# Kernel optimization log

Hardware: AMD Instinct MI355X
Metric: run time of the kernel (lower is better)

The kernel has to match this reference:

```python
import jax, jax.numpy as jnp
import numpy as np

B = 4096
D = 1024
WEIGHT = 1.0
EPS = 1e-7  # Keras K.epsilon()


def setup_inputs() -> dict:
    key = jax.random.key(0)
    k1, k2 = jax.random.split(key)
    return {
        "left": jax.random.normal(k1, (B, D), dtype=jnp.float32),
        "right": jax.random.normal(k2, (B, D), dtype=jnp.float32),
        "temperature": jnp.zeros((1,), dtype=jnp.float32),
    }


def _l2_normalize(x):
    # matches l2_norm: sqrt(max(sum(x^2), eps))
    sq = jnp.sum(jnp.square(x), axis=-1, keepdims=True)
    return x / jnp.sqrt(jnp.maximum(sq, EPS))


def reference(left, right, temperature):
    ln = _l2_normalize(left)   # [B, D]
    rn = _l2_normalize(right)  # [B, D]
    scale = jnp.exp(temperature)  # (1,) broadcasts
    logits_left = jnp.einsum("bd,cd->bc", ln, rn) * scale   # [B, B]
    logits_right = logits_left.T                             # rn @ ln.T * scale
    prob_left = jax.nn.softmax(logits_left, axis=-1)
    prob_right = jax.nn.softmax(logits_right, axis=-1)
    # NOTE: the original calls CCE(prob, labels), i.e. y_true=prob, y_pred=eye.
    # Keras clips y_pred to [eps, 1-eps]; loss = -sum(y_true * log(clip(y_pred))).
    labels = jnp.eye(B, dtype=jnp.float32)
    log_clipped = jnp.log(jnp.clip(labels, EPS, 1.0 - EPS))  # diag: log(1-eps), off: log(eps)
    loss_left = -jnp.sum(prob_left * log_clipped)
    loss_right = -jnp.sum(prob_right * log_clipped)
    loss = (loss_left + loss_right) / 2.0 / B
    return WEIGHT * loss
```

## Files before the change

kernel.cpp:

```cpp
#include <hip/hip_runtime.h>
#include <hip/hip_bf16.h>

#define Bn 4096
#define Dk 1024
#define EPSF 1e-7f

typedef unsigned short ushort_t;
typedef __bf16 bf16x8 __attribute__((ext_vector_type(8)));
typedef float f32x4 __attribute__((ext_vector_type(4)));

__device__ __forceinline__ unsigned pack_bf16_2(float a, float b) {
    __hip_bfloat162 h = __float22bfloat162_rn(make_float2(a, b));
    unsigned u;
    __builtin_memcpy(&u, &h, 4);
    return u;
}

__device__ __forceinline__ void async_copy16(const void* g, void* l) {
    __builtin_amdgcn_global_load_lds((__attribute__((address_space(1))) void*)(uintptr_t)g,
                                     (__attribute__((address_space(3))) void*)l, 16, 0, 0);
}

__global__ __launch_bounds__(256)
void nrm_kernel(const float4* __restrict__ left, const float4* __restrict__ right,
                uint2* __restrict__ lnb, uint2* __restrict__ rnb,
                float* __restrict__ diag, float* __restrict__ rowsum,
                float* __restrict__ colsum)
{
    const int row = blockIdx.x;
    const int t = threadIdx.x;
    const int idx = row * (Dk / 4) + t;
    const float4 l = left[idx];
    const float4 r = right[idx];
    float sl = l.x * l.x + l.y * l.y + l.z * l.z + l.w * l.w;
    float sr = r.x * r.x + r.y * r.y + r.z * r.z + r.w * r.w;
    float slr = l.x * r.x + l.y * r.y + l.z * r.z + l.w * r.w;
    #pragma unroll
    for (int off = 1; off < 64; off <<= 1) {
        sl += __shfl_xor(sl, off);
        sr += __shfl_xor(sr, off);
        slr += __shfl_xor(slr, off);
    }
    __shared__ float red[3][4];
    const int wave = t >> 6, lane = t & 63;
    if (lane == 0) { red[0][wave] = sl; red[1][wave] = sr; red[2][wave] = slr; }
    __syncthreads();
    sl = red[0][0] + red[0][1] + red[0][2] + red[0][3];
    sr = red[1][0] + red[1][1] + red[1][2] + red[1][3];
    const float invl = 1.0f / sqrtf(fmaxf(sl, EPSF));
    const float invr = 1.0f / sqrtf(fmaxf(sr, EPSF));
    lnb[idx] = make_uint2(pack_bf16_2(l.x * invl, l.y * invl),
                          pack_bf16_2(l.z * invl, l.w * invl));
    rnb[idx] = make_uint2(pack_bf16_2(r.x * invr, r.y * invr),
                          pack_bf16_2(r.z * invr, r.w * invr));
    if (t == 0) {
        const float d = red[2][0] + red[2][1] + red[2][2] + red[2][3];
        diag[row] = d * invl * invr;
        rowsum[row] = 0.f;
        colsum[row] = 0.f;
    }
}

__global__ __launch_bounds__(256, 2)
void gemm_sm_kernel(const ushort_t* __restrict__ lnb, const ushort_t* __restrict__ rnb,
                    const float* __restrict__ temp,
                    float* __restrict__ rowsum, float* __restrict__ colsum)
{
    __shared__ __align__(16) ushort_t As[128 * 32];
    __shared__ __align__(16) ushort_t Bs[128 * 32];

    const int tid = threadIdx.x;
    const int wave = tid >> 6;
    const int lane = tid & 63;
    const int bm0 = blockIdx.y * 128;
    const int bn0 = blockIdx.x * 128;

    const int srow = wave * 32 + (lane >> 2);
    const int scol = (lane & 3) * 8;
    const ushort_t* gA0 = lnb + (size_t)(bm0 + srow) * Dk + scol;
    const ushort_t* gA1 = gA0 + 16 * Dk;
    const ushort_t* gB0 = rnb + (size_t)(bn0 + srow) * Dk + scol;
    const ushort_t* gB1 = gB0 + 16 * Dk;
    ushort_t* lA0 = &As[(wave * 32) * 32];
    ushort_t* lA1 = lA0 + 16 * 32;
    ushort_t* lB0 = &Bs[(wave * 32) * 32];
    ushort_t* lB1 = lB0 + 16 * 32;

    const int wm = (wave & 1) * 64;
    const int wn = (wave >> 1) * 64;
    const int quad = lane >> 4;
    const int r16 = lane & 15;

    f32x4 acc[4][4];
    #pragma unroll
    for (int i = 0; i < 4; ++i)
        #pragma unroll
        for (int j = 0; j < 4; ++j)
            acc[i][j] = (f32x4){0.f, 0.f, 0.f, 0.f};

    int aoff[4], boff[4];
    #pragma unroll
    for (int i = 0; i < 4; ++i) {
        aoff[i] = (wm + i * 16 + r16) * 32 + quad * 8;
        boff[i] = (wn + i * 16 + r16) * 32 + quad * 8;
    }

    for (int k0 = 0; k0 < Dk; k0 += 32) {
        async_copy16(gA0 + k0, lA0);
        async_copy16(gA1 + k0, lA1);
        async_copy16(gB0 + k0, lB0);
        async_copy16(gB1 + k0, lB1);
        __syncthreads();
        bf16x8 af[4], bfv[4];
        #pragma unroll
        for (int i = 0; i < 4; ++i) af[i] = *(const bf16x8*)(&As[aoff[i]]);
        #pragma unroll
        for (int i = 0; i < 4; ++i) bfv[i] = *(const bf16x8*)(&Bs[boff[i]]);
        #pragma unroll
        for (int mi = 0; mi < 4; ++mi)
            #pragma unroll
            for (int ni = 0; ni < 4; ++ni)
                acc[mi][ni] = __builtin_amdgcn_mfma_f32_16x16x32_bf16(
                    af[mi], bfv[ni], acc[mi][ni], 0, 0, 0);
        __syncthreads();
    }

    const float scale = __expf(temp[0]);
    #pragma unroll
    for (int mi = 0; mi < 4; ++mi)
        #pragma unroll
        for (int ni = 0; ni < 4; ++ni)
            #pragma unroll
            for (int r = 0; r < 4; ++r)
                acc[mi][ni][r] = __expf(scale * acc[mi][ni][r] - scale);

    #pragma unroll
    for (int mi = 0; mi < 4; ++mi) {
        #pragma unroll
        for (int r = 0; r < 4; ++r) {
            float v = acc[mi][0][r] + acc[mi][1][r] + acc[mi][2][r] + acc[mi][3][r];
            v += __shfl_xor(v, 1);
            v += __shfl_xor(v, 2);
            v += __shfl_xor(v, 4);
            v += __shfl_xor(v, 8);
            if (r16 == 0)
                atomicAdd(&rowsum[bm0 + wm + mi * 16 + quad * 4 + r], v);
        }
    }
    #pragma unroll
    for (int ni = 0; ni < 4; ++ni) {
        float v = 0.f;
        #pragma unroll
        for (int mi = 0; mi < 4; ++mi)
            #pragma unroll
            for (int r = 0; r < 4; ++r)
                v += acc[mi][ni][r];
        v += __shfl_xor(v, 16);
        v += __shfl_xor(v, 32);
        if (quad == 0)
            atomicAdd(&colsum[bn0 + wn + ni * 16 + r16], v);
    }
}

__global__ __launch_bounds__(256)
void loss_kernel(const float* __restrict__ diag, const float* __restrict__ rowsum,
                 const float* __restrict__ colsum, const float* __restrict__ temp,
                 float* __restrict__ out)
{
    const int t = threadIdx.x;
    const float scale = __expf(temp[0]);
    float dL = 0.f, dR = 0.f;
    for (int i = t; i < Bn; i += 256) {
        const float e = __expf(scale * (diag[i] - 1.0f));
        dL += e / rowsum[i];
        dR += e / colsum[i];
    }
    #pragma unroll
    for (int off = 1; off < 64; off <<= 1) {
        dL += __shfl_xor(dL, off);
        dR += __shfl_xor(dR, off);
    }
    __shared__ float rd[2][4];
    const int wave = t >> 6, lane = t & 63;
    if (lane == 0) { rd[0][wave] = dL; rd[1][wave] = dR; }
    __syncthreads();
    if (t == 0) {
        dL = rd[0][0] + rd[0][1] + rd[0][2] + rd[0][3];
        dR = rd[1][0] + rd[1][1] + rd[1][2] + rd[1][3];
        const float logeps = logf(EPSF);
        const float log1m = logf(1.0f - EPSF);
        const float lossL = -(dL * log1m + ((float)Bn - dL) * logeps);
        const float lossR = -(dR * log1m + ((float)Bn - dR) * logeps);
        out[0] = (lossL + lossR) * 0.5f / (float)Bn;
    }
}

extern "C" void kernel_launch(void* const* d_in, const int* in_sizes, int n_in,
                              void* d_out, int out_size, void* d_ws, size_t ws_size,
                              hipStream_t stream) {
    (void)in_sizes; (void)n_in; (void)out_size; (void)ws_size;
    const float* left = (const float*)d_in[0];
    const float* right = (const float*)d_in[1];
    const float* temp = (const float*)d_in[2];

    char* ws = (char*)d_ws;
    ushort_t* lnb = (ushort_t*)ws;
    ushort_t* rnb = (ushort_t*)(ws + (size_t)Bn * Dk * sizeof(ushort_t));
    float* diag = (float*)(ws + (size_t)Bn * Dk * 4);
    float* rowsum = diag + Bn;
    float* colsum = rowsum + Bn;

    nrm_kernel<<<Bn, 256, 0, stream>>>((const float4*)left, (const float4*)right,
                                       (uint2*)lnb, (uint2*)rnb, diag, rowsum, colsum);
    dim3 g2(Bn / 128, Bn / 128);
    gemm_sm_kernel<<<g2, 256, 0, stream>>>(lnb, rnb, temp, rowsum, colsum);
    loss_kernel<<<1, 256, 0, stream>>>(diag, rowsum, colsum, temp, (float*)d_out);
}
```

Baseline: 130.9 us.

## Switch similarity GEMM from bf16 to scaled fp8 MFMA with swizzled LDS tiles

Normalized rows are now quantized to fp8 (pre-scaled by 8, undone via the MFMA scale exponents) instead of bf16. The GEMM uses the 16x16x128 f8f6f4 scaled MFMA with a K-step of 128 and XOR-swizzled LDS layout. This halves operand memory traffic and raises matrix throughput, at the cost of lower precision in the logits. The final loss kernel also swaps division for a hardware reciprocal.

```diff
diff --git a/kernel.cpp b/kernel.cpp
--- a/kernel.cpp
+++ b/kernel.cpp
@@ -5,16 +5,9 @@
 #define Dk 1024
 #define EPSF 1e-7f
 
-typedef unsigned short ushort_t;
-typedef __bf16 bf16x8 __attribute__((ext_vector_type(8)));
+typedef int i32x4 __attribute__((ext_vector_type(4)));
+typedef int i32x8 __attribute__((ext_vector_type(8)));
 typedef float f32x4 __attribute__((ext_vector_type(4)));
-
-__device__ __forceinline__ unsigned pack_bf16_2(float a, float b) {
-    __hip_bfloat162 h = __float22bfloat162_rn(make_float2(a, b));
-    unsigned u;
-    __builtin_memcpy(&u, &h, 4);
-    return u;
-}
 
 __device__ __forceinline__ void async_copy16(const void* g, void* l) {
     __builtin_amdgcn_global_load_lds((__attribute__((address_space(1))) void*)(uintptr_t)g,
@@ -23,7 +16,7 @@
 
 __global__ __launch_bounds__(256)
 void nrm_kernel(const float4* __restrict__ left, const float4* __restrict__ right,
-                uint2* __restrict__ lnb, uint2* __restrict__ rnb,
+                unsigned* __restrict__ lnb8, unsigned* __restrict__ rnb8,
                 float* __restrict__ diag, float* __restrict__ rowsum,
                 float* __restrict__ colsum)
 {
@@ -49,10 +42,14 @@
     sr = red[1][0] + red[1][1] + red[1][2] + red[1][3];
     const float invl = 1.0f / sqrtf(fmaxf(sl, EPSF));
     const float invr = 1.0f / sqrtf(fmaxf(sr, EPSF));
-    lnb[idx] = make_uint2(pack_bf16_2(l.x * invl, l.y * invl),
-                          pack_bf16_2(l.z * invl, l.w * invl));
-    rnb[idx] = make_uint2(pack_bf16_2(r.x * invr, r.y * invr),
-                          pack_bf16_2(r.z * invr, r.w * invr));
+    const float sL = 8.0f * invl;
+    const float sR = 8.0f * invr;
+    int pkL = __builtin_amdgcn_cvt_pk_fp8_f32(l.x * sL, l.y * sL, 0, false);
+    pkL = __builtin_amdgcn_cvt_pk_fp8_f32(l.z * sL, l.w * sL, pkL, true);
+    int pkR = __builtin_amdgcn_cvt_pk_fp8_f32(r.x * sR, r.y * sR, 0, false);
+    pkR = __builtin_amdgcn_cvt_pk_fp8_f32(r.z * sR, r.w * sR, pkR, true);
+    lnb8[idx] = (unsigned)pkL;
+    rnb8[idx] = (unsigned)pkR;
     if (t == 0) {
         const float d = red[2][0] + red[2][1] + red[2][2] + red[2][3];
         diag[row] = d * invl * invr;
@@ -62,12 +59,13 @@
 }
 
 __global__ __launch_bounds__(256, 2)
-void gemm_sm_kernel(const ushort_t* __restrict__ lnb, const ushort_t* __restrict__ rnb,
+void gemm_sm_kernel(const unsigned char* __restrict__ lnb8,
+                    const unsigned char* __restrict__ rnb8,
                     const float* __restrict__ temp,
                     float* __restrict__ rowsum, float* __restrict__ colsum)
 {
-    __shared__ __align__(16) ushort_t As[128 * 32];
-    __shared__ __align__(16) ushort_t Bs[128 * 32];
+    __shared__ __align__(16) unsigned char As[128 * 128];
+    __shared__ __align__(16) unsigned char Bs[128 * 128];
 
     const int tid = threadIdx.x;
     const int wave = tid >> 6;
@@ -75,21 +73,36 @@
     const int bm0 = blockIdx.y * 128;
     const int bn0 = blockIdx.x * 128;
 
-    const int srow = wave * 32 + (lane >> 2);
-    const int scol = (lane & 3) * 8;
-    const ushort_t* gA0 = lnb + (size_t)(bm0 + srow) * Dk + scol;
-    const ushort_t* gA1 = gA0 + 16 * Dk;
-    const ushort_t* gB0 = rnb + (size_t)(bn0 + srow) * Dk + scol;
-    const ushort_t* gB1 = gB0 + 16 * Dk;
-    ushort_t* lA0 = &As[(wave * 32) * 32];
-    ushort_t* lA1 = lA0 + 16 * 32;
-    ushort_t* lB0 = &Bs[(wave * 32) * 32];
-    ushort_t* lB1 = lB0 + 16 * 32;
+    const int lr = lane >> 3;
+    const int lc = lane & 7;
+    const int gcol = (lc ^ lr) * 16;
+    const unsigned char* gA[4];
+    const unsigned char* gB[4];
+    unsigned char* lA[4];
+    unsigned char* lB[4];
+    #pragma unroll
+    for (int c8 = 0; c8 < 4; ++c8) {
+        const int rloc = wave * 32 + c8 * 8;
+        gA[c8] = lnb8 + (size_t)(bm0 + rloc + lr) * Dk + gcol;
+        gB[c8] = rnb8 + (size_t)(bn0 + rloc + lr) * Dk + gcol;
+        lA[c8] = As + rloc * 128;
+        lB[c8] = Bs + rloc * 128;
+    }
 
     const int wm = (wave & 1) * 64;
     const int wn = (wave >> 1) * 64;
     const int quad = lane >> 4;
     const int r16 = lane & 15;
+    const int key = r16 & 7;
+    const int c0 = ((quad * 2) ^ key) * 16;
+    const int c1 = ((quad * 2 + 1) ^ key) * 16;
+
+    int arow[4], brow[4];
+    #pragma unroll
+    for (int i = 0; i < 4; ++i) {
+        arow[i] = (wm + i * 16 + r16) * 128;
+        brow[i] = (wn + i * 16 + r16) * 128;
+    }
 
     f32x4 acc[4][4];
     #pragma unroll
@@ -98,30 +111,34 @@
         for (int j = 0; j < 4; ++j)
             acc[i][j] = (f32x4){0.f, 0.f, 0.f, 0.f};
 
-    int aoff[4], boff[4];
-    #pragma unroll
-    for (int i = 0; i < 4; ++i) {
-        aoff[i] = (wm + i * 16 + r16) * 32 + quad * 8;
-        boff[i] = (wn + i * 16 + r16) * 32 + quad * 8;
-    }
-
-    for (int k0 = 0; k0 < Dk; k0 += 32) {
-        async_copy16(gA0 + k0, lA0);
-        async_copy16(gA1 + k0, lA1);
-        async_copy16(gB0 + k0, lB0);
-        async_copy16(gB1 + k0, lB1);
+    for (int k0 = 0; k0 < Dk; k0 += 128) {
+        #pragma unroll
+        for (int c8 = 0; c8 < 4; ++c8) {
+            async_copy16(gA[c8] + k0, lA[c8]);
+            async_copy16(gB[c8] + k0, lB[c8]);
+        }
         __syncthreads();
-        bf16x8 af[4], bfv[4];
-        #pragma unroll
-        for (int i = 0; i < 4; ++i) af[i] = *(const bf16x8*)(&As[aoff[i]]);
-        #pragma unroll
-        for (int i = 0; i < 4; ++i) bfv[i] = *(const bf16x8*)(&Bs[boff[i]]);
+        i32x8 af[4], bfv[4];
+        #pragma unroll
+        for (int i = 0; i < 4; ++i) {
+            const i32x4 lo = *(const i32x4*)(As + arow[i] + c0);
+            const i32x4 hi = *(const i32x4*)(As + arow[i] + c1);
+            af[i] = __builtin_shufflevector(lo, hi, 0, 1, 2, 3, 4, 5, 6, 7);
+        }
+        #pragma unroll
+        for (int i = 0; i < 4; ++i) {
+            const i32x4 lo = *(const i32x4*)(Bs + brow[i] + c0);
+            const i32x4 hi = *(const i32x4*)(Bs + brow[i] + c1);
+            bfv[i] = __builtin_shufflevector(lo, hi, 0, 1, 2, 3, 4, 5, 6, 7);
+        }
         #pragma unroll
         for (int mi = 0; mi < 4; ++mi)
             #pragma unroll
             for (int ni = 0; ni < 4; ++ni)
-                acc[mi][ni] = __builtin_amdgcn_mfma_f32_16x16x32_bf16(
-                    af[mi], bfv[ni], acc[mi][ni], 0, 0, 0);
+                acc[mi][ni] = __builtin_amdgcn_mfma_scale_f32_16x16x128_f8f6f4(
+                    af[mi], bfv[ni], acc[mi][ni], 0, 0,
+                    0, 124,
+                    0, 124);
         __syncthreads();
     }
 
@@ -172,8 +189,8 @@
     float dL = 0.f, dR = 0.f;
     for (int i = t; i < Bn; i += 256) {
         const float e = __expf(scale * (diag[i] - 1.0f));
-        dL += e / rowsum[i];
-        dR += e / colsum[i];
+        dL += e * __builtin_amdgcn_rcpf(rowsum[i]);
+        dR += e * __builtin_amdgcn_rcpf(colsum[i]);
     }
     #pragma unroll
     for (int off = 1; off < 64; off <<= 1) {
@@ -204,15 +221,15 @@
     const float* temp = (const float*)d_in[2];
 
     char* ws = (char*)d_ws;
-    ushort_t* lnb = (ushort_t*)ws;
-    ushort_t* rnb = (ushort_t*)(ws + (size_t)Bn * Dk * sizeof(ushort_t));
-    float* diag = (float*)(ws + (size_t)Bn * Dk * 4);
+    unsigned char* lnb8 = (unsigned char*)ws;
+    unsigned char* rnb8 = (unsigned char*)(ws + (size_t)Bn * Dk);
+    float* diag = (float*)(ws + 2 * (size_t)Bn * Dk);
     float* rowsum = diag + Bn;
     float* colsum = rowsum + Bn;
 
     nrm_kernel<<<Bn, 256, 0, stream>>>((const float4*)left, (const float4*)right,
-                                       (uint2*)lnb, (uint2*)rnb, diag, rowsum, colsum);
+                                       (unsigned*)lnb8, (unsigned*)rnb8, diag, rowsum, colsum);
     dim3 g2(Bn / 128, Bn / 128);
-    gemm_sm_kernel<<<g2, 256, 0, stream>>>(lnb, rnb, temp, rowsum, colsum);
+    gemm_sm_kernel<<<g2, 256, 0, stream>>>(lnb8, rnb8, temp, rowsum, colsum);
     loss_kernel<<<1, 256, 0, stream>>>(diag, rowsum, colsum, temp, (float*)d_out);
 }
```

Measured after the change: 187.8 us. +43.4%, slower.
